# Optimization experiments

Hardware: AMD Instinct MI355X
Metric: run time of the kernel (lower is better)

Reference implementation:

```python
import jax, jax.numpy as jnp
import numpy as np

D_MODEL = 1024
NUM_HEADS = 16
HEAD_DIM = D_MODEL // NUM_HEADS


def setup_inputs() -> dict:
    key = jax.random.key(0)
    ks = jax.random.split(key, 9)
    s = 1.0 / np.sqrt(D_MODEL)
    x = jax.random.normal(ks[0], (2, 2048, D_MODEL), dtype=jnp.float32)
    Wq = jax.random.uniform(ks[1], (D_MODEL, D_MODEL), jnp.float32, -s, s)
    bq = jax.random.uniform(ks[2], (D_MODEL,), jnp.float32, -s, s)
    Wk = jax.random.uniform(ks[3], (D_MODEL, D_MODEL), jnp.float32, -s, s)
    bk = jax.random.uniform(ks[4], (D_MODEL,), jnp.float32, -s, s)
    Wv = jax.random.uniform(ks[5], (D_MODEL, D_MODEL), jnp.float32, -s, s)
    bv = jax.random.uniform(ks[6], (D_MODEL,), jnp.float32, -s, s)
    Wo = jax.random.uniform(ks[7], (D_MODEL, D_MODEL), jnp.float32, -s, s)
    bo = jax.random.uniform(ks[8], (D_MODEL,), jnp.float32, -s, s)
    return {"x": x, "Wq": Wq, "bq": bq, "Wk": Wk, "bk": bk,
            "Wv": Wv, "bv": bv, "Wo": Wo, "bo": bo}


def reference(x, Wq, bq, Wk, bk, Wv, bv, Wo, bo):
    B, S, _ = x.shape
    def split_heads(t):  # [B,S,D] -> [B,H,S,hd]
        return t.reshape(B, S, NUM_HEADS, HEAD_DIM).transpose(0, 2, 1, 3)
    q = split_heads(x @ Wq + bq)
    k = split_heads(x @ Wk + bk)
    v = split_heads(x @ Wv + bv)
    scores = jnp.einsum('bhqd,bhkd->bhqk', q, k) / np.sqrt(HEAD_DIM)
    attn = jax.nn.softmax(scores, axis=-1)
    ctx = jnp.einsum('bhqk,bhkd->bhqd', attn, v)
    ctx = ctx.transpose(0, 2, 1, 3).reshape(B, S, D_MODEL)
    return ctx @ Wo + bo
```

## Files before the change

kernel.cpp:

```cpp
#include <hip/hip_runtime.h>
#include <stdint.h>

#define DM 1024
#define SEQ 2048
#define NTOK 4096
#define HD 64

typedef __bf16 bf16x8 __attribute__((ext_vector_type(8)));
typedef float f32x4 __attribute__((ext_vector_type(4)));
typedef uint32_t u32x2 __attribute__((ext_vector_type(2)));
typedef uint32_t u32x4 __attribute__((ext_vector_type(4)));

#if __has_builtin(__builtin_amdgcn_exp2f)
#define EXP2F(x) __builtin_amdgcn_exp2f(x)
#else
#define EXP2F(x) exp2f(x)
#endif

__device__ __forceinline__ void gll16f(const char* g, char* lds_wave_base, int lane) {
#if __has_builtin(__builtin_amdgcn_global_load_lds)
  __builtin_amdgcn_global_load_lds(
      (const __attribute__((address_space(1))) void*)g,
      (__attribute__((address_space(3))) void*)lds_wave_base, 16, 0, 0);
#else
  *(bf16x8*)(lds_wave_base + lane * 16) = *(const bf16x8*)g;
#endif
}

__device__ __forceinline__ uint16_t f2bf(float f) {
  uint32_t x = __float_as_uint(f);
  return (uint16_t)((x + 0x7fffu + ((x >> 16) & 1u)) >> 16);
}

__device__ __forceinline__ uint32_t cvtpk(float a, float b) {
  uint32_t r;
  asm("v_cvt_pk_bf16_f32 %0, %1, %2" : "=v"(r) : "v"(a), "v"(b));
  return r;
}

__device__ __forceinline__ bf16x8 mk8(uint32_t a, uint32_t b, uint32_t c, uint32_t d) {
  u32x4 t = {a, b, c, d};
  return __builtin_bit_cast(bf16x8, t);
}

__global__ void prep_kernel(const float* __restrict__ x, uint16_t* __restrict__ xb,
                            const float* __restrict__ W0, const float* __restrict__ W1,
                            const float* __restrict__ W2, const float* __restrict__ W3,
                            uint16_t* __restrict__ T0, uint16_t* __restrict__ T1,
                            uint16_t* __restrict__ T2, uint16_t* __restrict__ T3) {
  __shared__ float t[32][33];
  int bid = blockIdx.x;
  if (bid < 4096) {
    int i = (bid * 256 + threadIdx.x) * 4;
    float4 v = *(const float4*)&x[i];
    uint64_t pk = (uint64_t)f2bf(v.x) | ((uint64_t)f2bf(v.y) << 16) |
                  ((uint64_t)f2bf(v.z) << 32) | ((uint64_t)f2bf(v.w) << 48);
    *(uint64_t*)&xb[i] = pk;
    return;
  }
  int b2 = bid - 4096;
  int zz = b2 >> 10, rr = b2 & 1023;
  const float* W = (zz == 0) ? W0 : (zz == 1) ? W1 : (zz == 2) ? W2 : W3;
  uint16_t* T = (zz == 0) ? T0 : (zz == 1) ? T1 : (zz == 2) ? T2 : T3;
  int tx = threadIdx.x & 31, ty = threadIdx.x >> 5;
  int nb = (rr & 31) * 32, kb = (rr >> 5) * 32;
#pragma unroll
  for (int i = 0; i < 4; i++)
    t[ty + i * 8][tx] = W[(kb + ty + i * 8) * DM + nb + tx];
  __syncthreads();
#pragma unroll
  for (int i = 0; i < 4; i++)
    T[(nb + ty + i * 8) * DM + kb + tx] = f2bf(t[tx][ty + i * 8]);
}

template <int MODE, int MF>
__device__ __forceinline__ void gemm_body(const uint16_t* __restrict__ A,
                                          const uint16_t* __restrict__ Bt,
                                          const float* __restrict__ bias, float scale,
                                          void* __restrict__ out, uint16_t* lds,
                                          int bx, int by) {
  const int tid = threadIdx.x;
  const int w = tid >> 6, lane = tid & 63;
  const int wr = w >> 1, wc = w & 1;
  const int a15 = lane & 15, a4 = lane >> 4;
  const int m0 = by * (MF * 32), n0 = bx * 128;
  char* lgA = (char*)lds;
  char* lgB = (char*)(lds + MF * 2048);
  f32x4 acc[MF][4];
#pragma unroll
  for (int m = 0; m < MF; m++)
#pragma unroll
    for (int n = 0; n < 4; n++) acc[m][n] = (f32x4){0.f, 0.f, 0.f, 0.f};

  const char* Ag = (const char*)(A + (size_t)m0 * DM);
  const char* Bg = (const char*)(Bt + (size_t)n0 * DM);
  const int srow = lane >> 3;
  const int scol = ((lane & 7) * 16) ^ (srow << 4);
  const int swz = (a15 & 7) << 4;

  for (int k0 = 0; k0 < DM; k0 += 64) {
#pragma unroll
    for (int c = 0; c < MF; c++) {
      int ro = w * (MF * 8) + c * 8 + srow;
      gll16f(Ag + (size_t)ro * (DM * 2) + k0 * 2 + scol, lgA + (w * MF + c) * 1024, lane);
    }
#pragma unroll
    for (int c = 0; c < 4; c++) {
      int ro = w * 32 + c * 8 + srow;
      gll16f(Bg + (size_t)ro * (DM * 2) + k0 * 2 + scol, lgB + (w * 4 + c) * 1024, lane);
    }
    __syncthreads();
    bf16x8 af[MF][2], bfr[4][2];
#pragma unroll
    for (int m = 0; m < MF; m++)
#pragma unroll
      for (int kk = 0; kk < 2; kk++)
        af[m][kk] = *(const bf16x8*)(lgA + (wr * (MF * 16) + m * 16 + a15) * 128 +
                                     ((kk * 64 + a4 * 16) ^ swz));
#pragma unroll
    for (int n = 0; n < 4; n++)
#pragma unroll
      for (int kk = 0; kk < 2; kk++)
        bfr[n][kk] = *(const bf16x8*)(lgB + (wc * 64 + n * 16 + a15) * 128 +
                                      ((kk * 64 + a4 * 16) ^ swz));
#pragma unroll
    for (int kk = 0; kk < 2; kk++)
#pragma unroll
      for (int m = 0; m < MF; m++)
#pragma unroll
        for (int n = 0; n < 4; n++)
          acc[m][n] = __builtin_amdgcn_mfma_f32_16x16x32_bf16(af[m][kk], bfr[n][kk],
                                                              acc[m][n], 0, 0, 0);
    __syncthreads();
  }

#pragma unroll
  for (int m = 0; m < MF; m++) {
#pragma unroll
    for (int n = 0; n < 4; n++) {
      int gr0 = m0 + wr * (MF * 16) + m * 16 + a4 * 4;
      int col = n0 + wc * 64 + n * 16 + a15;
      float bv = bias[col];
      if constexpr (MODE == 2) {
        float* O = (float*)out;
#pragma unroll
        for (int j = 0; j < 4; j++)
          O[(size_t)(gr0 + j) * DM + col] = acc[m][n][j] + bv;
      } else if constexpr (MODE == 0) {
        uint16_t* O = (uint16_t*)out;
        int h = col >> 6, d = col & 63;
#pragma unroll
        for (int j = 0; j < 4; j++) {
          int gr = gr0 + j;
          int b = gr >> 11, s = gr & 2047;
          O[((size_t)(((b << 4) + h)) * SEQ + s) * HD + d] = f2bf((acc[m][n][j] + bv) * scale);
        }
      } else {
        uint16_t* O = (uint16_t*)out;
        int h = col >> 6, d = col & 63;
        int b = gr0 >> 11, s0 = gr0 & 2047;
        int it = s0 >> 6, s6 = s0 & 63;
        int pos = (s6 >> 5) * 32 + ((s6 >> 2) & 3) * 8 + ((s6 >> 4) & 1) * 4;
        uint64_t pk = 0;
#pragma unroll
        for (int j = 0; j < 4; j++)
          pk |= (uint64_t)f2bf(acc[m][n][j] + bv) << (16 * j);
        *(uint64_t*)&O[((size_t)(((b << 4) + h)) * HD + d) * SEQ + it * 64 + pos] = pk;
      }
    }
  }
}

#define CS_SCALE 0.180336880f

__global__ __launch_bounds__(256, 2) void gemm_qkv_kernel(
    const uint16_t* __restrict__ xb, const uint16_t* __restrict__ wtq,
    const uint16_t* __restrict__ wtk, const uint16_t* __restrict__ wtv,
    const float* __restrict__ bq, const float* __restrict__ bk,
    const float* __restrict__ bv, uint16_t* __restrict__ qo,
    uint16_t* __restrict__ ko, uint16_t* __restrict__ vto) {
  __shared__ __attribute__((aligned(16))) uint16_t lds[16384];
  int id = blockIdx.x;
  int swz = (id & 7) * 96 + (id >> 3);
  int z = swz >> 8, r = swz & 255;
  int by = r >> 3, bx = r & 7;
  if (z == 0)      gemm_body<0, 4>(xb, wtq, bq, CS_SCALE, qo, lds, bx, by);
  else if (z == 1) gemm_body<0, 4>(xb, wtk, bk, 1.0f, ko, lds, bx, by);
  else             gemm_body<1, 4>(xb, wtv, bv, 1.0f, vto, lds, bx, by);
}

__global__ __launch_bounds__(256, 2) void gemm_out_kernel(
    const uint16_t* __restrict__ ctx, const uint16_t* __restrict__ wto,
    const float* __restrict__ bo, float* __restrict__ out) {
  __shared__ __attribute__((aligned(16))) uint16_t lds[12288];
  int id = blockIdx.x;
  int swz = (id & 7) * 64 + (id >> 3);
  int by = swz >> 3, bx = swz & 7;
  gemm_body<2, 2>(ctx, wto, bo, 1.0f, out, lds, bx, by);
}

__global__ __launch_bounds__(256, 2) void attn_kernel(
    const uint16_t* __restrict__ qg, const uint16_t* __restrict__ kg,
    const uint16_t* __restrict__ vtg, uint16_t* __restrict__ ctx) {
  const int tid = threadIdx.x;
  const int w = tid >> 6, l = tid & 63;
  const int l15 = l & 15, g = l >> 4;
  int id = blockIdx.x;
  int wg = (id & 7) * 64 + (id >> 3);
  int bh = wg >> 4, qb = wg & 15;
  const int q0 = qb * 128 + w * 32;
  const uint16_t* Qb = qg + (size_t)bh * SEQ * HD;
  const char* Kc = (const char*)(kg + (size_t)bh * SEQ * HD);
  const char* Vc = (const char*)(vtg + (size_t)bh * HD * SEQ);

  __shared__ __attribute__((aligned(16))) char Klds[4][8192];
  __shared__ __attribute__((aligned(16))) char Vlds[4][8192];

  const int srow = l >> 3;
  const int scolx = ((l & 7) * 16) ^ (srow << 4);

#define STAGE(BI, IT)                                                          \
  {                                                                            \
    const int it1_ = (IT);                                                     \
    _Pragma("unroll") for (int i = 0; i < 2; i++) {                            \
      int r = w * 16 + i * 8 + srow;                                           \
      gll16f(Kc + (size_t)(it1_ * 64 + r) * 128 + scolx,                       \
             &Klds[BI][w * 2048 + i * 1024], l);                               \
      gll16f(Vc + (size_t)r * (SEQ * 2) + it1_ * 128 + scolx,                  \
             &Vlds[BI][w * 2048 + i * 1024], l);                               \
    }                                                                          \
  }

  bf16x8 bq[2][2];
#pragma unroll
  for (int qs = 0; qs < 2; qs++)
#pragma unroll
    for (int ks = 0; ks < 2; ks++)
      bq[qs][ks] = *(const bf16x8*)&Qb[(size_t)(q0 + qs * 16 + l15) * HD + ks * 32 + g * 8];

  f32x4 o[4][2];
#pragma unroll
  for (int dt = 0; dt < 4; dt++)
#pragma unroll
    for (int qs = 0; qs < 2; qs++) o[dt][qs] = (f32x4){0.f, 0.f, 0.f, 0.f};
  f32x4 ol0 = {0.f, 0.f, 0.f, 0.f}, ol1 = {0.f, 0.f, 0.f, 0.f};
  const int swz = (l15 & 7) << 4;
  const uint32_t ONE2 = 0x3F803F80u;
  const bf16x8 aones = mk8(ONE2, ONE2, ONE2, ONE2);

#define TILE_BODY(BI)                                                          \
  {                                                                            \
                                            \
    bf16x8 ak[4][2];                                                           \
    _Pragma("unroll") for (int kt = 0; kt < 4; kt++)                           \
        _Pragma("unroll") for (int ks = 0; ks < 2; ks++)                       \
            ak[kt][ks] = *(const bf16x8*)&Klds[BI][(kt * 16 + l15) * 128 +     \
                                                   ((ks * 64 + g * 16) ^ swz)];\
                     \
    bf16x8 av[4][2];                                                           \
    _Pragma("unroll") for (int dt = 0; dt < 4; dt++)                           \
        _Pragma("unroll") for (int kb = 0; kb < 2; kb++)                       \
            av[dt][kb] = *(const bf16x8*)&Vlds[BI][(dt * 16 + l15) * 128 +     \
                                                   ((kb * 64 + g * 16) ^ swz)];\
                                           \
    f32x4 s[2][4];                                                             \
    _Pragma("unroll") for (int qs = 0; qs < 2; qs++)                           \
        _Pragma("unroll") for (int kt = 0; kt < 4; kt++)                       \
            s[qs][kt] = (f32x4){0.f, 0.f, 0.f, 0.f};                           \
    __builtin_amdgcn_s_setprio(1);                                             \
    _Pragma("unroll") for (int kt = 0; kt < 4; kt++)                           \
        _Pragma("unroll") for (int ks = 0; ks < 2; ks++) {                     \
      s[0][kt] = __builtin_amdgcn_mfma_f32_16x16x32_bf16(ak[kt][ks], bq[0][ks], s[0][kt], 0, 0, 0); \
      s[1][kt] = __builtin_amdgcn_mfma_f32_16x16x32_bf16(ak[kt][ks], bq[1][ks], s[1][kt], 0, 0, 0); \
    }                                                                          \
    __builtin_amdgcn_s_setprio(0);                                             \
        \
    float p0[4][4], p1[4][4];                                                  \
    _Pragma("unroll") for (int kt = 0; kt < 4; kt++)                           \
        _Pragma("unroll") for (int j = 0; j < 4; j++) {                        \
      p0[kt][j] = EXP2F(s[0][kt][j]);                                          \
      p1[kt][j] = EXP2F(s[1][kt][j]);                                          \
    }                                                                          \
    bf16x8 bp0[2], bp1[2];                                                     \
    _Pragma("unroll") for (int kb = 0; kb < 2; kb++) {                         \
      bp0[kb] = mk8(cvtpk(p0[2 * kb][0], p0[2 * kb][1]),                       \
                    cvtpk(p0[2 * kb][2], p0[2 * kb][3]),                       \
                    cvtpk(p0[2 * kb + 1][0], p0[2 * kb + 1][1]),               \
                    cvtpk(p0[2 * kb + 1][2], p0[2 * kb + 1][3]));              \
      bp1[kb] = mk8(cvtpk(p1[2 * kb][0], p1[2 * kb][1]),                       \
                    cvtpk(p1[2 * kb][2], p1[2 * kb][3]),                       \
                    cvtpk(p1[2 * kb + 1][0], p1[2 * kb + 1][1]),               \
                    cvtpk(p1[2 * kb + 1][2], p1[2 * kb + 1][3]));              \
    }                                                                          \
                                                \
    __builtin_amdgcn_s_setprio(1);                                             \
    _Pragma("unroll") for (int dt = 0; dt < 4; dt++)                           \
        _Pragma("unroll") for (int kb = 0; kb < 2; kb++) {                     \
      o[dt][0] = __builtin_amdgcn_mfma_f32_16x16x32_bf16(av[dt][kb], bp0[kb], o[dt][0], 0, 0, 0); \
      o[dt][1] = __builtin_amdgcn_mfma_f32_16x16x32_bf16(av[dt][kb], bp1[kb], o[dt][1], 0, 0, 0); \
    }                                                                          \
    _Pragma("unroll") for (int kb = 0; kb < 2; kb++) {                         \
      ol0 = __builtin_amdgcn_mfma_f32_16x16x32_bf16(aones, bp0[kb], ol0, 0, 0, 0); \
      ol1 = __builtin_amdgcn_mfma_f32_16x16x32_bf16(aones, bp1[kb], ol1, 0, 0, 0); \
    }                                                                          \
    __builtin_amdgcn_s_setprio(0);                                             \
  }

  STAGE(0, 0);
  STAGE(1, 1);

  for (int it4 = 0; it4 < 8; ++it4) {
    int tb = it4 * 4;
    STAGE(2, tb + 2);
    STAGE(3, tb + 3);
    asm volatile("s_waitcnt vmcnt(8)\n\ts_barrier" ::: "memory");
    TILE_BODY(0);
    TILE_BODY(1);
    asm volatile("s_waitcnt lgkmcnt(0)\n\ts_barrier" ::: "memory");
    if (it4 < 7) {
      STAGE(0, tb + 4);
      STAGE(1, tb + 5);
      asm volatile("s_waitcnt vmcnt(8)\n\ts_barrier" ::: "memory");
    } else {
      asm volatile("s_waitcnt vmcnt(0)\n\ts_barrier" ::: "memory");
    }
    TILE_BODY(2);
    TILE_BODY(3);
    asm volatile("s_waitcnt lgkmcnt(0)\n\ts_barrier" ::: "memory");
  }
#undef TILE_BODY
#undef STAGE

  float inv0 = 1.0f / ol0[0];
  float inv1 = 1.0f / ol1[0];
  int b = bh >> 4, h = bh & 15;
  uint16_t* cr0 = ctx + (size_t)(b * SEQ + q0 + l15) * DM + h * HD + 4 * g;
  uint16_t* cr1 = cr0 + (size_t)16 * DM;
#pragma unroll
  for (int dt = 0; dt < 4; dt++) {
    u32x2 wv;
    wv[0] = cvtpk(o[dt][0][0] * inv0, o[dt][0][1] * inv0);
    wv[1] = cvtpk(o[dt][0][2] * inv0, o[dt][0][3] * inv0);
    *(u32x2*)&cr0[dt * 16] = wv;
    u32x2 wv2;
    wv2[0] = cvtpk(o[dt][1][0] * inv1, o[dt][1][1] * inv1);
    wv2[1] = cvtpk(o[dt][1][2] * inv1, o[dt][1][3] * inv1);
    *(u32x2*)&cr1[dt * 16] = wv2;
  }
}

extern "C" void kernel_launch(void* const* d_in, const int* in_sizes, int n_in,
                              void* d_out, int out_size, void* d_ws, size_t ws_size,
                              hipStream_t stream) {
  const float* x  = (const float*)d_in[0];
  const float* Wq = (const float*)d_in[1];
  const float* bq = (const float*)d_in[2];
  const float* Wk = (const float*)d_in[3];
  const float* bk = (const float*)d_in[4];
  const float* Wv = (const float*)d_in[5];
  const float* bv = (const float*)d_in[6];
  const float* Wo = (const float*)d_in[7];
  const float* bo = (const float*)d_in[8];

  char* ws = (char*)d_ws;
  uint16_t* xb  = (uint16_t*)(ws);
  uint16_t* wtq = (uint16_t*)(ws + 8388608);
  uint16_t* wtk = (uint16_t*)(ws + 10485760);
  uint16_t* wtv = (uint16_t*)(ws + 12582912);
  uint16_t* wto = (uint16_t*)(ws + 14680064);
  uint16_t* qb  = (uint16_t*)(ws + 16777216);
  uint16_t* kb  = (uint16_t*)(ws + 25165824);
  uint16_t* vtb = (uint16_t*)(ws + 33554432);
  uint16_t* ctx = xb;

  prep_kernel<<<dim3(8192), dim3(256), 0, stream>>>(
      x, xb, Wq, Wk, Wv, Wo, wtq, wtk, wtv, wto);
  gemm_qkv_kernel<<<dim3(768), dim3(256), 0, stream>>>(
      xb, wtq, wtk, wtv, bq, bk, bv, qb, kb, vtb);
  attn_kernel<<<dim3(512), dim3(256), 0, stream>>>(qb, kb, vtb, ctx);
  gemm_out_kernel<<<dim3(512), dim3(256), 0, stream>>>(ctx, wto, bo, (float*)d_out);
}
```

Baseline: 92.18 us.

## Load V fragments directly from global into registers, double-buffer K in LDS

The attention kernel stops staging V through LDS. Each lane now loads its V^T fragments straight from global memory into registers one tile ahead, using two register sets. K staging drops from four LDS buffers to two, with one barrier pair per 64-key tile instead of per four tiles. This frees LDS and removes the LDS read traffic for V, but it adds register pressure, loses the deeper prefetch, and adds more barriers. It also relies on the vmcnt(10) wait count matching the number of outstanding loads.

Measured after the change: 126.0 us. 36.7% more time.

```diff
diff --git a/kernel.cpp b/kernel.cpp
--- a/kernel.cpp
+++ b/kernel.cpp
@@ -211,10 +211,9 @@
   const int q0 = qb * 128 + w * 32;
   const uint16_t* Qb = qg + (size_t)bh * SEQ * HD;
   const char* Kc = (const char*)(kg + (size_t)bh * SEQ * HD);
-  const char* Vc = (const char*)(vtg + (size_t)bh * HD * SEQ);
-
-  __shared__ __attribute__((aligned(16))) char Klds[4][8192];
-  __shared__ __attribute__((aligned(16))) char Vlds[4][8192];
+  const uint16_t* Vg = vtg + (size_t)bh * HD * SEQ + (size_t)l15 * SEQ + g * 8;
+
+  __shared__ __attribute__((aligned(16))) char Klds[2][8192];
 
   const int srow = l >> 3;
   const int scolx = ((l & 7) * 16) ^ (srow << 4);
@@ -226,9 +225,16 @@
       int r = w * 16 + i * 8 + srow;                                           \
       gll16f(Kc + (size_t)(it1_ * 64 + r) * 128 + scolx,                       \
              &Klds[BI][w * 2048 + i * 1024], l);                               \
-      gll16f(Vc + (size_t)r * (SEQ * 2) + it1_ * 128 + scolx,                  \
-             &Vlds[BI][w * 2048 + i * 1024], l);                               \
-    }                                                                          \
+    }                                                                          \
+  }
+
+#define VLOAD(AV, IT)                                                          \
+  {                                                                            \
+    const int itv_ = (IT);                                                     \
+    _Pragma("unroll") for (int dt = 0; dt < 4; dt++)                           \
+        _Pragma("unroll") for (int kb = 0; kb < 2; kb++)                       \
+            AV[dt][kb] = *(const bf16x8*)&Vg[(size_t)dt * 16 * SEQ +           \
+                                             itv_ * 64 + kb * 32];             \
   }
 
   bf16x8 bq[2][2];
@@ -248,20 +254,24 @@
   const uint32_t ONE2 = 0x3F803F80u;
   const bf16x8 aones = mk8(ONE2, ONE2, ONE2, ONE2);
 
-#define TILE_BODY(BI)                                                          \
+  bf16x8 avA[4][2], avB[4][2];
+
+#define TILE(IT, BI, BN, AVC, AVN)                                             \
   {                                                                            \
+    const int it_ = (IT);                                                      \
+    if (it_ + 1 < SEQ / 64) {                                                  \
+      VLOAD(AVN, it_ + 1);                                                     \
+      STAGE(BN, it_ + 1);                                                      \
+      asm volatile("s_waitcnt vmcnt(10)\n\ts_barrier" ::: "memory");           \
+    } else {                                                                   \
+      asm volatile("s_waitcnt vmcnt(0)\n\ts_barrier" ::: "memory");            \
+    }                                                                          \
                                             \
     bf16x8 ak[4][2];                                                           \
     _Pragma("unroll") for (int kt = 0; kt < 4; kt++)                           \
         _Pragma("unroll") for (int ks = 0; ks < 2; ks++)                       \
             ak[kt][ks] = *(const bf16x8*)&Klds[BI][(kt * 16 + l15) * 128 +     \
                                                    ((ks * 64 + g * 16) ^ swz)];\
-                     \
-    bf16x8 av[4][2];                                                           \
-    _Pragma("unroll") for (int dt = 0; dt < 4; dt++)                           \
-        _Pragma("unroll") for (int kb = 0; kb < 2; kb++)                       \
-            av[dt][kb] = *(const bf16x8*)&Vlds[BI][(dt * 16 + l15) * 128 +     \
-                                                   ((kb * 64 + g * 16) ^ swz)];\
                                            \
     f32x4 s[2][4];                                                             \
     _Pragma("unroll") for (int qs = 0; qs < 2; qs++)                           \
@@ -296,39 +306,27 @@
     __builtin_amdgcn_s_setprio(1);                                             \
     _Pragma("unroll") for (int dt = 0; dt < 4; dt++)                           \
         _Pragma("unroll") for (int kb = 0; kb < 2; kb++) {                     \
-      o[dt][0] = __builtin_amdgcn_mfma_f32_16x16x32_bf16(av[dt][kb], bp0[kb], o[dt][0], 0, 0, 0); \
-      o[dt][1] = __builtin_amdgcn_mfma_f32_16x16x32_bf16(av[dt][kb], bp1[kb], o[dt][1], 0, 0, 0); \
+      o[dt][0] = __builtin_amdgcn_mfma_f32_16x16x32_bf16(AVC[dt][kb], bp0[kb], o[dt][0], 0, 0, 0); \
+      o[dt][1] = __builtin_amdgcn_mfma_f32_16x16x32_bf16(AVC[dt][kb], bp1[kb], o[dt][1], 0, 0, 0); \
     }                                                                          \
     _Pragma("unroll") for (int kb = 0; kb < 2; kb++) {                         \
       ol0 = __builtin_amdgcn_mfma_f32_16x16x32_bf16(aones, bp0[kb], ol0, 0, 0, 0); \
       ol1 = __builtin_amdgcn_mfma_f32_16x16x32_bf16(aones, bp1[kb], ol1, 0, 0, 0); \
     }                                                                          \
     __builtin_amdgcn_s_setprio(0);                                             \
-  }
-
+    asm volatile("s_waitcnt lgkmcnt(0)\n\ts_barrier" ::: "memory");            \
+  }
+
+  VLOAD(avA, 0);
   STAGE(0, 0);
-  STAGE(1, 1);
-
-  for (int it4 = 0; it4 < 8; ++it4) {
-    int tb = it4 * 4;
-    STAGE(2, tb + 2);
-    STAGE(3, tb + 3);
-    asm volatile("s_waitcnt vmcnt(8)\n\ts_barrier" ::: "memory");
-    TILE_BODY(0);
-    TILE_BODY(1);
-    asm volatile("s_waitcnt lgkmcnt(0)\n\ts_barrier" ::: "memory");
-    if (it4 < 7) {
-      STAGE(0, tb + 4);
-      STAGE(1, tb + 5);
-      asm volatile("s_waitcnt vmcnt(8)\n\ts_barrier" ::: "memory");
-    } else {
-      asm volatile("s_waitcnt vmcnt(0)\n\ts_barrier" ::: "memory");
-    }
-    TILE_BODY(2);
-    TILE_BODY(3);
-    asm volatile("s_waitcnt lgkmcnt(0)\n\ts_barrier" ::: "memory");
-  }
-#undef TILE_BODY
+  asm volatile("s_waitcnt vmcnt(0)\n\ts_barrier" ::: "memory");
+
+  for (int it2 = 0; it2 < SEQ / 128; ++it2) {
+    TILE(2 * it2, 0, 1, avA, avB);
+    TILE(2 * it2 + 1, 1, 0, avB, avA);
+  }
+#undef TILE
+#undef VLOAD
 #undef STAGE
 
   float inv0 = 1.0f / ol0[0];
```
